# Kernel optimization log

Hardware: AMD Instinct MI355X
Metric: run time of the kernel (lower is better)

The kernel has to match this reference:

```python
import jax, jax.numpy as jnp
import numpy as np
from math import pi

BS, H, C = 4096, 1024, 512
H2, C2 = H // 2, C // 2


def _cm(x, y):
    # complex multiply with real/imag stored in last dim
    return jnp.stack([x[..., 0] * y[..., 0] - x[..., 1] * y[..., 1],
                      x[..., 0] * y[..., 1] + x[..., 1] * y[..., 0]], -1)


def _interleave(a, b):
    # (H2, C2),(H2, C2) -> (H, C2) rows [a0,b0,a1,b1,...]
    return jnp.stack([a, b], 1).reshape(-1, a.shape[1])


def _rotations(phi, theta):
    cp, sp = jnp.cos(phi), jnp.sin(phi)
    ct, st = jnp.cos(theta), jnp.sin(theta)
    z = jnp.zeros_like(ct)
    diag = jnp.stack([_interleave(cp * ct, ct), _interleave(sp * ct, z)], -1)      # (H, C2, 2)
    offd = jnp.stack([_interleave(-cp * st, st), _interleave(-sp * st, z)], -1)    # (H, C2, 2)
    return diag.transpose(1, 0, 2), offd.transpose(1, 0, 2)                        # (C2, H, 2)


def _swap_pairs(x):
    # swap elements within adjacent pairs along the hidden axis
    bs, h, _ = x.shape
    return x.reshape(bs, h // 2, 2, 2)[:, :, ::-1, :].reshape(bs, h, 2)


def setup_inputs() -> dict:
    key = jax.random.key(0)
    ks = jax.random.split(key, 5)
    x = jax.random.normal(ks[0], (BS, H, 2), dtype=jnp.float32)
    phi0 = 2 * pi * jax.random.normal(ks[1], (H2, C2), dtype=jnp.float32)
    theta0 = 2 * pi * jax.random.normal(ks[2], (H2, C2), dtype=jnp.float32)
    phi1 = 2 * pi * jax.random.normal(ks[3], (H2, C2), dtype=jnp.float32)
    theta1 = 2 * pi * jax.random.normal(ks[4], (H2, C2), dtype=jnp.float32)
    return {"x": x, "phi0": phi0, "theta0": theta0, "phi1": phi1, "theta1": theta1}


def reference(x, phi0, theta0, phi1, theta1):
    d0, o0 = _rotations(phi0, theta0)
    d1, o1 = _rotations(phi1, theta1)

    def step(xc, dd):
        dd0, oo0, dd1, oo1 = dd
        xc = _cm(xc, dd0) + _cm(_swap_pairs(xc), oo0)
        xc = jnp.roll(xc, -1, axis=1)   # cat(x[1:], x[:1])
        xc = _cm(xc, dd1) + _cm(_swap_pairs(xc), oo1)
        xc = jnp.roll(xc, 1, axis=1)    # cat(x[-1:], x[:-1])
        return xc, None

    x, _ = jax.lax.scan(step, x, (d0, o0, d1, o1))
    return x
```

## Files before the change

kernel.cpp:

```cpp
#include <hip/hip_runtime.h>


#define H_DIM 1024
#define C2 256
#define RPW 4


__global__ __launch_bounds__(256) void eunn_coef_kernel(
    const float* __restrict__ phi0, const float* __restrict__ theta0,
    const float* __restrict__ phi1, const float* __restrict__ theta1,
    float4* __restrict__ coef) {
    int t = blockIdx.x * 256 + threadIdx.x;
    int i = t & 511;
    int p = (t >> 9) & 1;
    int c = t >> 10;
    const float* phi   = p ? phi1   : phi0;
    const float* theta = p ? theta1 : theta0;
    float ph = phi[i * C2 + c];
    float th = theta[i * C2 + c];
    float sp, cp, st, ct;
    __sincosf(ph, &sp, &cp);
    __sincosf(th, &st, &ct);
    int j = i & 7;
    int l = i >> 3;
    coef[(((c * 2 + p) * 8) + j) * 64 + l] = make_float4(ct, st, cp, sp);
}

__device__ __forceinline__ void rot_pair(const float4 q,
                                         float& ur, float& ui,
                                         float& wr, float& wi) {
    float ar = fmaf(-q.y, wr, q.x * ur);
    float ai = fmaf(-q.y, wi, q.x * ui);
    float br = fmaf( q.x, wr, q.y * ur);
    float bi = fmaf( q.x, wi, q.y * ui);
    ur = fmaf(-q.w, ai, q.z * ar);
    ui = fmaf( q.w, ar, q.z * ai);
    wr = br;
    wi = bi;
}

__global__ __launch_bounds__(256, 1) void eunn_main_kernel(
    const float* __restrict__ x,
    const float4* __restrict__ coef,
    float* __restrict__ out) {
    const int lane = threadIdx.x & 63;
    const int wave = threadIdx.x >> 6;
    const int row0 = (blockIdx.x * 4 + wave) * RPW;
    const int lnext = (lane + 1) & 63;
    const int lprev = (lane + 63) & 63;

    float vr[RPW][16], vi[RPW][16];

#pragma unroll
    for (int r = 0; r < RPW; ++r) {
        const float4* src = (const float4*)(x + (size_t)(row0 + r) * (H_DIM * 2)) + lane * 8;
#pragma unroll
        for (int m = 0; m < 8; ++m) {
            float4 f = src[m];
            vr[r][2 * m]     = f.x; vi[r][2 * m]     = f.y;
            vr[r][2 * m + 1] = f.z; vi[r][2 * m + 1] = f.w;
        }
    }

    const float4* cl = coef + lane;

    float4 A[8], B[8];
#pragma unroll
    for (int j = 0; j < 8; ++j) A[j] = cl[j * 64];

#pragma unroll 1
    for (int c = 0; c < C2; ++c) {
        const float4* cb = cl + (size_t)c * 1024;

#pragma unroll
        for (int j = 0; j < 8; ++j) B[j] = cb[(8 + j) * 64];
        __builtin_amdgcn_sched_barrier(0);

#pragma unroll
        for (int j = 0; j < 8; ++j) {
#pragma unroll
            for (int r = 0; r < RPW; ++r)
                rot_pair(A[j], vr[r][2 * j],     vi[r][2 * j],
                               vr[r][2 * j + 1], vi[r][2 * j + 1]);
        }

        float4 qq = B[7];
        float qpx = __shfl(qq.x, lprev);
        float qpy = __shfl(qq.y, lprev);
        float nbr[RPW], nbi[RPW], pbr[RPW], pbi[RPW];
#pragma unroll
        for (int r = 0; r < RPW; ++r) {
            nbr[r] = __shfl(vr[r][0],  lnext);
            nbi[r] = __shfl(vi[r][0],  lnext);
            pbr[r] = __shfl(vr[r][15], lprev);
            pbi[r] = __shfl(vi[r][15], lprev);
        }

        const int cn = (c + 1 < C2) ? (c + 1) : 0;
        const float4* cnp = cl + (size_t)cn * 1024;
#pragma unroll
        for (int j = 0; j < 8; ++j) A[j] = cnp[j * 64];
        __builtin_amdgcn_sched_barrier(0);

#pragma unroll
        for (int j = 0; j < 7; ++j) {
#pragma unroll
            for (int r = 0; r < RPW; ++r)
                rot_pair(B[j], vr[r][2 * j + 1], vi[r][2 * j + 1],
                               vr[r][2 * j + 2], vi[r][2 * j + 2]);
        }

#pragma unroll
        for (int r = 0; r < RPW; ++r) {
            float ar = fmaf(-qq.y, nbr[r], qq.x * vr[r][15]);
            float ai = fmaf(-qq.y, nbi[r], qq.x * vi[r][15]);
            vr[r][15] = fmaf(-qq.w, ai, qq.z * ar);
            vi[r][15] = fmaf( qq.w, ar, qq.z * ai);
            float b0r = fmaf(qpx, vr[r][0], qpy * pbr[r]);
            float b0i = fmaf(qpx, vi[r][0], qpy * pbi[r]);
            vr[r][0] = b0r; vi[r][0] = b0i;
        }
    }

#pragma unroll
    for (int r = 0; r < RPW; ++r) {
        float4* dst = (float4*)(out + (size_t)(row0 + r) * (H_DIM * 2)) + lane * 8;
#pragma unroll
        for (int m = 0; m < 8; ++m) {
            dst[m] = make_float4(vr[r][2 * m],     vi[r][2 * m],
                                 vr[r][2 * m + 1], vi[r][2 * m + 1]);
        }
    }
}

extern "C" void kernel_launch(void* const* d_in, const int* in_sizes, int n_in,
                              void* d_out, int out_size, void* d_ws, size_t ws_size,
                              hipStream_t stream) {
    const float* x      = (const float*)d_in[0];
    const float* phi0   = (const float*)d_in[1];
    const float* theta0 = (const float*)d_in[2];
    const float* phi1   = (const float*)d_in[3];
    const float* theta1 = (const float*)d_in[4];
    float* out = (float*)d_out;
    float4* coef = (float4*)d_ws;

    hipLaunchKernelGGL(eunn_coef_kernel, dim3(1024), dim3(256), 0, stream,
                       phi0, theta0, phi1, theta1, coef);

    hipLaunchKernelGGL(eunn_main_kernel, dim3(256), dim3(256), 0, stream,
                       x, coef, out);
}
```

Before: 457.5 us.

## Halve rows per wave, double grid, and software-pipeline coefficient loads in groups

Each wave now processes two rows instead of four, and the grid doubles to 512 blocks with launch bounds allowing two blocks per CU, so more waves can hide latency. Coefficient loads are restructured into groups of four float4 loads issued ahead of the rotations that consume them, with empty asm pins and memory fences to enforce the ordering, and the first group for the next column is prefetched. The shuffles and boundary rotations are interleaved with independent work. This trades less per-wave coefficient reuse (each coefficient is loaded for fewer rows) for higher occupancy and finer-grained overlap of loads with math.

```diff
diff --git a/kernel.cpp b/kernel.cpp
--- a/kernel.cpp
+++ b/kernel.cpp
@@ -3,7 +3,7 @@
 
 #define H_DIM 1024
 #define C2 256
-#define RPW 4
+#define RPW 2
 
 
 __global__ __launch_bounds__(256) void eunn_coef_kernel(
@@ -39,7 +39,24 @@
     wi = bi;
 }
 
-__global__ __launch_bounds__(256, 1) void eunn_main_kernel(
+
+#define ROT2(q, e0, e1)                                                  \
+    do {                                                                 \
+        _Pragma("unroll")                                                \
+        for (int r = 0; r < RPW; ++r)                                    \
+            rot_pair(q, vr[r][e0], vi[r][e0], vr[r][e1], vi[r][e1]);     \
+    } while (0)
+
+#define PIN4(a, b, c, d)                                                 \
+    asm volatile(""                                                      \
+        : "+v"(a.x), "+v"(a.y), "+v"(a.z), "+v"(a.w),                    \
+          "+v"(b.x), "+v"(b.y), "+v"(b.z), "+v"(b.w),                    \
+          "+v"(c.x), "+v"(c.y), "+v"(c.z), "+v"(c.w),                    \
+          "+v"(d.x), "+v"(d.y), "+v"(d.z), "+v"(d.w))
+
+#define MEMFENCE asm volatile("" ::: "memory")
+
+__global__ __launch_bounds__(256, 2) void eunn_main_kernel(
     const float* __restrict__ x,
     const float4* __restrict__ coef,
     float* __restrict__ out) {
@@ -64,29 +81,21 @@
 
     const float4* cl = coef + lane;
 
-    float4 A[8], B[8];
-#pragma unroll
-    for (int j = 0; j < 8; ++j) A[j] = cl[j * 64];
+    float4 pA0 = cl[0 * 64], pA7 = cl[7 * 64], pQQ = cl[15 * 64], pA1 = cl[1 * 64];
 
 #pragma unroll 1
     for (int c = 0; c < C2; ++c) {
         const float4* cb = cl + (size_t)c * 1024;
+        const float4* cn = cl + (size_t)((c + 1) & (C2 - 1)) * 1024;
 
-#pragma unroll
-        for (int j = 0; j < 8; ++j) B[j] = cb[(8 + j) * 64];
-        __builtin_amdgcn_sched_barrier(0);
-
-#pragma unroll
-        for (int j = 0; j < 8; ++j) {
-#pragma unroll
-            for (int r = 0; r < RPW; ++r)
-                rot_pair(A[j], vr[r][2 * j],     vi[r][2 * j],
-                               vr[r][2 * j + 1], vi[r][2 * j + 1]);
-        }
-
-        float4 qq = B[7];
+        PIN4(pA0, pA7, pQQ, pA1);
+        float4 pA2 = cb[2 * 64], pA3 = cb[3 * 64], pA4 = cb[4 * 64], pA5 = cb[5 * 64];
+        MEMFENCE;
+        float4 qq = pQQ;
         float qpx = __shfl(qq.x, lprev);
         float qpy = __shfl(qq.y, lprev);
+        ROT2(pA0, 0, 1);
+        ROT2(pA7, 14, 15);
         float nbr[RPW], nbi[RPW], pbr[RPW], pbi[RPW];
 #pragma unroll
         for (int r = 0; r < RPW; ++r) {
@@ -95,20 +104,31 @@
             pbr[r] = __shfl(vr[r][15], lprev);
             pbi[r] = __shfl(vi[r][15], lprev);
         }
+        ROT2(pA1, 2, 3);
 
-        const int cn = (c + 1 < C2) ? (c + 1) : 0;
-        const float4* cnp = cl + (size_t)cn * 1024;
-#pragma unroll
-        for (int j = 0; j < 8; ++j) A[j] = cnp[j * 64];
-        __builtin_amdgcn_sched_barrier(0);
+        PIN4(pA2, pA3, pA4, pA5);
+        float4 pA6 = cb[6 * 64], pB0 = cb[8 * 64], pB1 = cb[9 * 64], pB2 = cb[10 * 64];
+        MEMFENCE;
+        ROT2(pA2, 4, 5);
+        ROT2(pA3, 6, 7);
+        ROT2(pA4, 8, 9);
+        ROT2(pA5, 10, 11);
 
-#pragma unroll
-        for (int j = 0; j < 7; ++j) {
-#pragma unroll
-            for (int r = 0; r < RPW; ++r)
-                rot_pair(B[j], vr[r][2 * j + 1], vi[r][2 * j + 1],
-                               vr[r][2 * j + 2], vi[r][2 * j + 2]);
-        }
+        PIN4(pA6, pB0, pB1, pB2);
+        float4 pB3 = cb[11 * 64], pB4 = cb[12 * 64], pB5 = cb[13 * 64], pB6 = cb[14 * 64];
+        MEMFENCE;
+        ROT2(pA6, 12, 13);
+        ROT2(pB0, 1, 2);
+        ROT2(pB1, 3, 4);
+        ROT2(pB2, 5, 6);
+
+        PIN4(pB3, pB4, pB5, pB6);
+        pA0 = cn[0 * 64]; pA7 = cn[7 * 64]; pQQ = cn[15 * 64]; pA1 = cn[1 * 64];
+        MEMFENCE;
+        ROT2(pB3, 7, 8);
+        ROT2(pB4, 9, 10);
+        ROT2(pB5, 11, 12);
+        ROT2(pB6, 13, 14);
 
 #pragma unroll
         for (int r = 0; r < RPW; ++r) {
@@ -147,6 +167,6 @@
     hipLaunchKernelGGL(eunn_coef_kernel, dim3(1024), dim3(256), 0, stream,
                        phi0, theta0, phi1, theta1, coef);
 
-    hipLaunchKernelGGL(eunn_main_kernel, dim3(256), dim3(256), 0, stream,
+    hipLaunchKernelGGL(eunn_main_kernel, dim3(512), dim3(256), 0, stream,
                        x, coef, out);
 }
```

After: 487.0 us. 1.06x slower.

## Split each row across two waves with LDS halo exchange per layer

Applied to the files above, without the earlier changes.

Each row of 1024 hidden elements is now split across two waves of 64 lanes, with 16 elements per lane. Each wave still processes 4 rows, and the grid grows to 1024 blocks of 128 threads. The boundary values at the wave edges are exchanged through shared memory, with a barrier every layer. The coefficient layout is reordered to match, and coefficient prefetch is double-buffered by unrolling two layers per loop. The aim is to raise the number of waves in flight and to halve per-thread register state, at the cost of an LDS exchange and a block barrier on every layer.

```diff
diff --git a/kernel.cpp b/kernel.cpp
--- a/kernel.cpp
+++ b/kernel.cpp
@@ -3,7 +3,6 @@
 
 #define H_DIM 1024
 #define C2 256
-#define RPW 4
 
 
 __global__ __launch_bounds__(256) void eunn_coef_kernel(
@@ -11,9 +10,12 @@
     const float* __restrict__ phi1, const float* __restrict__ theta1,
     float4* __restrict__ coef) {
     int t = blockIdx.x * 256 + threadIdx.x;
-    int i = t & 511;
-    int p = (t >> 9) & 1;
+    int l = t & 63;
+    int k = (t >> 6) & 3;
+    int p = (t >> 8) & 1;
+    int w = (t >> 9) & 1;
     int c = t >> 10;
+    int i = 256 * w + 4 * l + k;
     const float* phi   = p ? phi1   : phi0;
     const float* theta = p ? theta1 : theta0;
     float ph = phi[i * C2 + c];
@@ -21,9 +23,7 @@
     float sp, cp, st, ct;
     __sincosf(ph, &sp, &cp);
     __sincosf(th, &st, &ct);
-    int j = i & 7;
-    int l = i >> 3;
-    coef[(((c * 2 + p) * 8) + j) * 64 + l] = make_float4(ct, st, cp, sp);
+    coef[t] = make_float4(ct, st, cp, sp);
 }
 
 __device__ __forceinline__ void rot_pair(const float4 q,
@@ -39,96 +39,131 @@
     wi = bi;
 }
 
-__global__ __launch_bounds__(256, 1) void eunn_main_kernel(
+__global__ __launch_bounds__(128, 2) void eunn_main_kernel(
     const float* __restrict__ x,
     const float4* __restrict__ coef,
     float* __restrict__ out) {
     const int lane = threadIdx.x & 63;
-    const int wave = threadIdx.x >> 6;
-    const int row0 = (blockIdx.x * 4 + wave) * RPW;
+    const int w    = threadIdx.x >> 6;
+    const int row0 = blockIdx.x * 4;
     const int lnext = (lane + 1) & 63;
     const int lprev = (lane + 63) & 63;
 
-    float vr[RPW][16], vi[RPW][16];
+    __shared__ float4 ex[2][2][5];
+
+    float vr[4][8], vi[4][8];
 
 #pragma unroll
-    for (int r = 0; r < RPW; ++r) {
-        const float4* src = (const float4*)(x + (size_t)(row0 + r) * (H_DIM * 2)) + lane * 8;
+    for (int r = 0; r < 4; ++r) {
+        const float4* src = (const float4*)(x + (size_t)(row0 + r) * (H_DIM * 2))
+                            + (w * 256 + lane * 4);
 #pragma unroll
-        for (int m = 0; m < 8; ++m) {
-            float4 f = src[m];
-            vr[r][2 * m]     = f.x; vi[r][2 * m]     = f.y;
-            vr[r][2 * m + 1] = f.z; vi[r][2 * m + 1] = f.w;
+        for (int k = 0; k < 4; ++k) {
+            float4 f = src[k];
+            vr[r][2 * k]     = f.x; vi[r][2 * k]     = f.y;
+            vr[r][2 * k + 1] = f.z; vi[r][2 * k + 1] = f.w;
         }
     }
 
-    const float4* cl = coef + lane;
+    const float4* cl = coef + (w * 512 + lane);
 
-    float4 A[8], B[8];
+    float4 CA[4], CB[4], NA[4], NB[4];
 #pragma unroll
-    for (int j = 0; j < 8; ++j) A[j] = cl[j * 64];
+    for (int k = 0; k < 4; ++k) {
+        CA[k] = cl[k * 64];
+        CB[k] = cl[256 + k * 64];
+    }
+
+#define LAYER(CA_, CB_, NA_, NB_, cnext, par)                                      \
+    do {                                                                           \
+                    \
+        const float4* cn_ = cl + (size_t)(cnext) * 1024;                           \
+        _Pragma("unroll")                                                          \
+        for (int k = 0; k < 4; ++k) {                                              \
+            NA_[k] = cn_[k * 64];                                                  \
+            NB_[k] = cn_[256 + k * 64];                                            \
+        }                                                                          \
+        float4 qq = CB_[3];                                                        \
+        float qpx = __shfl(qq.x, lprev);                 \
+        float qpy = __shfl(qq.y, lprev);                 \
+                                        \
+        _Pragma("unroll")                                                          \
+        for (int k = 0; k < 4; ++k)                                                \
+            _Pragma("unroll")                                                      \
+            for (int r = 0; r < 4; ++r)                                            \
+                rot_pair(CA_[k], vr[r][2 * k],     vi[r][2 * k],                   \
+                                 vr[r][2 * k + 1], vi[r][2 * k + 1]);              \
+                 \
+        float nbr[4], nbi[4], pbr[4], pbi[4];                                      \
+        _Pragma("unroll")                                                          \
+        for (int r = 0; r < 4; ++r) {                                              \
+            nbr[r] = __shfl(vr[r][0], lnext);                                      \
+            nbi[r] = __shfl(vi[r][0], lnext);                                      \
+            pbr[r] = __shfl(vr[r][7], lprev);                                      \
+            pbi[r] = __shfl(vi[r][7], lprev);                                      \
+        }                                                                          \
+        if (lane == 0) {                                                           \
+            ex[par][w][0] = make_float4(vr[0][0], vi[0][0], vr[1][0], vi[1][0]);   \
+            ex[par][w][1] = make_float4(vr[2][0], vi[2][0], vr[3][0], vi[3][0]);   \
+        } else if (lane == 63) {                                                   \
+            ex[par][w][2] = make_float4(vr[0][7], vi[0][7], vr[1][7], vi[1][7]);   \
+            ex[par][w][3] = make_float4(vr[2][7], vi[2][7], vr[3][7], vi[3][7]);   \
+            ex[par][w][4] = make_float4(qq.x, qq.y, qq.x, qq.y);                   \
+        }                                                                          \
+              \
+        asm volatile("" ::: "memory");                                             \
+        asm volatile("s_waitcnt lgkmcnt(0)" ::: "memory");                         \
+        __builtin_amdgcn_s_barrier();                                              \
+        asm volatile("" ::: "memory");                                             \
+        {                                                                          \
+            float4 e0a = ex[par][w ^ 1][0], e0b = ex[par][w ^ 1][1];               \
+            float4 e7a = ex[par][w ^ 1][2], e7b = ex[par][w ^ 1][3];               \
+            float4 qpo = ex[par][w ^ 1][4];                                        \
+            if (lane == 63) {                                                      \
+                nbr[0] = e0a.x; nbi[0] = e0a.y; nbr[1] = e0a.z; nbi[1] = e0a.w;    \
+                nbr[2] = e0b.x; nbi[2] = e0b.y; nbr[3] = e0b.z; nbi[3] = e0b.w;    \
+            }                                                                      \
+            if (lane == 0) {                                                       \
+                pbr[0] = e7a.x; pbi[0] = e7a.y; pbr[1] = e7a.z; pbi[1] = e7a.w;    \
+                pbr[2] = e7b.x; pbi[2] = e7b.y; pbr[3] = e7b.z; pbi[3] = e7b.w;    \
+                qpx = qpo.x; qpy = qpo.y;                                          \
+            }                                                                      \
+        }                                                                          \
+                                 \
+        _Pragma("unroll")                                                          \
+        for (int k = 0; k < 3; ++k)                                                \
+            _Pragma("unroll")                                                      \
+            for (int r = 0; r < 4; ++r)                                            \
+                rot_pair(CB_[k], vr[r][2 * k + 1], vi[r][2 * k + 1],               \
+                                 vr[r][2 * k + 2], vi[r][2 * k + 2]);              \
+                                \
+        _Pragma("unroll")                                                          \
+        for (int r = 0; r < 4; ++r) {                                              \
+            float ar = fmaf(-qq.y, nbr[r], qq.x * vr[r][7]);                       \
+            float ai = fmaf(-qq.y, nbi[r], qq.x * vi[r][7]);                       \
+            vr[r][7] = fmaf(-qq.w, ai, qq.z * ar);                                 \
+            vi[r][7] = fmaf( qq.w, ar, qq.z * ai);                                 \
+            float b0r = fmaf(qpx, vr[r][0], qpy * pbr[r]);                         \
+            float b0i = fmaf(qpx, vi[r][0], qpy * pbi[r]);                         \
+            vr[r][0] = b0r; vi[r][0] = b0i;                                        \
+        }                                                                          \
+    } while (0)
 
 #pragma unroll 1
-    for (int c = 0; c < C2; ++c) {
-        const float4* cb = cl + (size_t)c * 1024;
+    for (int c = 0; c < C2; c += 2) {
+        LAYER(CA, CB, NA, NB, c + 1, 0);
+        LAYER(NA, NB, CA, CB, (c + 2) & (C2 - 1), 1);
+    }
+#undef LAYER
 
 #pragma unroll
-        for (int j = 0; j < 8; ++j) B[j] = cb[(8 + j) * 64];
-        __builtin_amdgcn_sched_barrier(0);
-
+    for (int r = 0; r < 4; ++r) {
+        float4* dst = (float4*)(out + (size_t)(row0 + r) * (H_DIM * 2))
+                      + (w * 256 + lane * 4);
 #pragma unroll
-        for (int j = 0; j < 8; ++j) {
-#pragma unroll
-            for (int r = 0; r < RPW; ++r)
-                rot_pair(A[j], vr[r][2 * j],     vi[r][2 * j],
-                               vr[r][2 * j + 1], vi[r][2 * j + 1]);
-        }
-
-        float4 qq = B[7];
-        float qpx = __shfl(qq.x, lprev);
-        float qpy = __shfl(qq.y, lprev);
-        float nbr[RPW], nbi[RPW], pbr[RPW], pbi[RPW];
-#pragma unroll
-        for (int r = 0; r < RPW; ++r) {
-            nbr[r] = __shfl(vr[r][0],  lnext);
-            nbi[r] = __shfl(vi[r][0],  lnext);
-            pbr[r] = __shfl(vr[r][15], lprev);
-            pbi[r] = __shfl(vi[r][15], lprev);
-        }
-
-        const int cn = (c + 1 < C2) ? (c + 1) : 0;
-        const float4* cnp = cl + (size_t)cn * 1024;
-#pragma unroll
-        for (int j = 0; j < 8; ++j) A[j] = cnp[j * 64];
-        __builtin_amdgcn_sched_barrier(0);
-
-#pragma unroll
-        for (int j = 0; j < 7; ++j) {
-#pragma unroll
-            for (int r = 0; r < RPW; ++r)
-                rot_pair(B[j], vr[r][2 * j + 1], vi[r][2 * j + 1],
-                               vr[r][2 * j + 2], vi[r][2 * j + 2]);
-        }
-
-#pragma unroll
-        for (int r = 0; r < RPW; ++r) {
-            float ar = fmaf(-qq.y, nbr[r], qq.x * vr[r][15]);
-            float ai = fmaf(-qq.y, nbi[r], qq.x * vi[r][15]);
-            vr[r][15] = fmaf(-qq.w, ai, qq.z * ar);
-            vi[r][15] = fmaf( qq.w, ar, qq.z * ai);
-            float b0r = fmaf(qpx, vr[r][0], qpy * pbr[r]);
-            float b0i = fmaf(qpx, vi[r][0], qpy * pbi[r]);
-            vr[r][0] = b0r; vi[r][0] = b0i;
-        }
-    }
-
-#pragma unroll
-    for (int r = 0; r < RPW; ++r) {
-        float4* dst = (float4*)(out + (size_t)(row0 + r) * (H_DIM * 2)) + lane * 8;
-#pragma unroll
-        for (int m = 0; m < 8; ++m) {
-            dst[m] = make_float4(vr[r][2 * m],     vi[r][2 * m],
-                                 vr[r][2 * m + 1], vi[r][2 * m + 1]);
+        for (int k = 0; k < 4; ++k) {
+            dst[k] = make_float4(vr[r][2 * k],     vi[r][2 * k],
+                                 vr[r][2 * k + 1], vi[r][2 * k + 1]);
         }
     }
 }
@@ -147,6 +182,6 @@
     hipLaunchKernelGGL(eunn_coef_kernel, dim3(1024), dim3(256), 0, stream,
                        phi0, theta0, phi1, theta1, coef);
 
-    hipLaunchKernelGGL(eunn_main_kernel, dim3(256), dim3(256), 0, stream,
+    hipLaunchKernelGGL(eunn_main_kernel, dim3(1024), dim3(128), 0, stream,
                        x, coef, out);
 }
```

After: 465.9 us. About the same (+1.8%).

## Halve rows per wave, double grid, and software-pipeline coef loads with inline asm

Applied to the files above, without the earlier changes.

Each wave now holds 2 rows instead of 4 and the grid doubles to 512 blocks, with waves_per_eu set to 2 so more waves are resident to hide latency. Coefficient loads are issued through inline-asm global_load_dwordx4 with immediate offsets and explicit vmcnt(0) drains. The next layer's loads overlap the current layer's rotation math, and the boundary shuffles are issued early between rotations. The trade-off is that each coefficient load is now amortised over fewer rows, which raises coefficient traffic, and the hand-placed waitcnts could serialise work.

```diff
diff --git a/kernel.cpp b/kernel.cpp
--- a/kernel.cpp
+++ b/kernel.cpp
@@ -3,7 +3,9 @@
 
 #define H_DIM 1024
 #define C2 256
-#define RPW 4
+#define RPW 2
+
+typedef float f4 __attribute__((ext_vector_type(4)));
 
 
 __global__ __launch_bounds__(256) void eunn_coef_kernel(
@@ -26,7 +28,7 @@
     coef[(((c * 2 + p) * 8) + j) * 64 + l] = make_float4(ct, st, cp, sp);
 }
 
-__device__ __forceinline__ void rot_pair(const float4 q,
+__device__ __forceinline__ void rot_pair(const f4 q,
                                          float& ur, float& ui,
                                          float& wr, float& wi) {
     float ar = fmaf(-q.y, wr, q.x * ur);
@@ -39,9 +41,28 @@
     wi = bi;
 }
 
-__global__ __launch_bounds__(256, 1) void eunn_main_kernel(
+#define GLOAD(dst, base, off)                                              \
+    asm volatile("global_load_dwordx4 %0, %1, off offset:" #off            \
+                 : "=v"(dst) : "v"(base))
+
+#define VMDRAIN                                                            \
+    do {                                                                   \
+        asm volatile("s_waitcnt vmcnt(0)");                                \
+        __builtin_amdgcn_sched_barrier(0);                                 \
+    } while (0)
+
+#define ROT2(q, e0, e1)                                                    \
+    do {                                                                   \
+        _Pragma("unroll")                                                  \
+        for (int r = 0; r < RPW; ++r)                                      \
+            rot_pair(q, vr[r][e0], vi[r][e0], vr[r][e1], vi[r][e1]);       \
+    } while (0)
+
+__global__ __launch_bounds__(256)
+__attribute__((amdgpu_waves_per_eu(2, 2)))
+void eunn_main_kernel(
     const float* __restrict__ x,
-    const float4* __restrict__ coef,
+    const f4* __restrict__ coef,
     float* __restrict__ out) {
     const int lane = threadIdx.x & 63;
     const int wave = threadIdx.x >> 6;
@@ -53,40 +74,42 @@
 
 #pragma unroll
     for (int r = 0; r < RPW; ++r) {
-        const float4* src = (const float4*)(x + (size_t)(row0 + r) * (H_DIM * 2)) + lane * 8;
+        const f4* src = (const f4*)(x + (size_t)(row0 + r) * (H_DIM * 2)) + lane * 8;
 #pragma unroll
         for (int m = 0; m < 8; ++m) {
-            float4 f = src[m];
+            f4 f = src[m];
             vr[r][2 * m]     = f.x; vi[r][2 * m]     = f.y;
             vr[r][2 * m + 1] = f.z; vi[r][2 * m + 1] = f.w;
         }
     }
 
-    const float4* cl = coef + lane;
+    const f4* cl = coef + lane;
 
-    float4 A[8], B[8];
-#pragma unroll
-    for (int j = 0; j < 8; ++j) A[j] = cl[j * 64];
+    f4 A0, A1, A2, A3, A4, A5, A6, A7;
+    f4 B0, B1, B2, B3, B4, B5, B6, B7;
+
+    {
+        const f4* g0 = cl;
+        const f4* g1 = cl + 256;
+        GLOAD(A0, g0, 0); GLOAD(A1, g0, 1024); GLOAD(A2, g0, 2048); GLOAD(A3, g0, 3072);
+        GLOAD(A4, g1, 0); GLOAD(A5, g1, 1024); GLOAD(A6, g1, 2048); GLOAD(A7, g1, 3072);
+    }
+    VMDRAIN;
 
 #pragma unroll 1
     for (int c = 0; c < C2; ++c) {
-        const float4* cb = cl + (size_t)c * 1024;
+        const f4* cb = cl + (size_t)c * 1024;
+        const f4* cn = cl + (size_t)((c + 1) & (C2 - 1)) * 1024;
 
-#pragma unroll
-        for (int j = 0; j < 8; ++j) B[j] = cb[(8 + j) * 64];
-        __builtin_amdgcn_sched_barrier(0);
-
-#pragma unroll
-        for (int j = 0; j < 8; ++j) {
-#pragma unroll
-            for (int r = 0; r < RPW; ++r)
-                rot_pair(A[j], vr[r][2 * j],     vi[r][2 * j],
-                               vr[r][2 * j + 1], vi[r][2 * j + 1]);
+        {
+            const f4* g2 = cb + 512;
+            const f4* g3 = cb + 768;
+            GLOAD(B0, g2, 0); GLOAD(B1, g2, 1024); GLOAD(B2, g2, 2048); GLOAD(B3, g2, 3072);
+            GLOAD(B4, g3, 0); GLOAD(B5, g3, 1024); GLOAD(B6, g3, 2048); GLOAD(B7, g3, 3072);
         }
 
-        float4 qq = B[7];
-        float qpx = __shfl(qq.x, lprev);
-        float qpy = __shfl(qq.y, lprev);
+        ROT2(A0, 0, 1);
+        ROT2(A7, 14, 15);
         float nbr[RPW], nbi[RPW], pbr[RPW], pbi[RPW];
 #pragma unroll
         for (int r = 0; r < RPW; ++r) {
@@ -95,40 +118,56 @@
             pbr[r] = __shfl(vr[r][15], lprev);
             pbi[r] = __shfl(vi[r][15], lprev);
         }
+        ROT2(A1, 2, 3);
+        ROT2(A2, 4, 5);
+        ROT2(A3, 6, 7);
+        ROT2(A4, 8, 9);
+        ROT2(A5, 10, 11);
+        ROT2(A6, 12, 13);
 
-        const int cn = (c + 1 < C2) ? (c + 1) : 0;
-        const float4* cnp = cl + (size_t)cn * 1024;
-#pragma unroll
-        for (int j = 0; j < 8; ++j) A[j] = cnp[j * 64];
-        __builtin_amdgcn_sched_barrier(0);
+        VMDRAIN;
 
-#pragma unroll
-        for (int j = 0; j < 7; ++j) {
-#pragma unroll
-            for (int r = 0; r < RPW; ++r)
-                rot_pair(B[j], vr[r][2 * j + 1], vi[r][2 * j + 1],
-                               vr[r][2 * j + 2], vi[r][2 * j + 2]);
+        float qpx = __shfl(B7.x, lprev);
+        float qpy = __shfl(B7.y, lprev);
+
+        {
+            const f4* g0 = cn;
+            const f4* g1 = cn + 256;
+            GLOAD(A0, g0, 0); GLOAD(A1, g0, 1024); GLOAD(A2, g0, 2048); GLOAD(A3, g0, 3072);
+            GLOAD(A4, g1, 0); GLOAD(A5, g1, 1024); GLOAD(A6, g1, 2048); GLOAD(A7, g1, 3072);
         }
+
+        ROT2(B0, 1, 2);
+        ROT2(B1, 3, 4);
+        ROT2(B2, 5, 6);
+        ROT2(B3, 7, 8);
+        ROT2(B4, 9, 10);
+        ROT2(B5, 11, 12);
+        ROT2(B6, 13, 14);
 
 #pragma unroll
         for (int r = 0; r < RPW; ++r) {
-            float ar = fmaf(-qq.y, nbr[r], qq.x * vr[r][15]);
-            float ai = fmaf(-qq.y, nbi[r], qq.x * vi[r][15]);
-            vr[r][15] = fmaf(-qq.w, ai, qq.z * ar);
-            vi[r][15] = fmaf( qq.w, ar, qq.z * ai);
+            float ar = fmaf(-B7.y, nbr[r], B7.x * vr[r][15]);
+            float ai = fmaf(-B7.y, nbi[r], B7.x * vi[r][15]);
+            vr[r][15] = fmaf(-B7.w, ai, B7.z * ar);
+            vi[r][15] = fmaf( B7.w, ar, B7.z * ai);
             float b0r = fmaf(qpx, vr[r][0], qpy * pbr[r]);
             float b0i = fmaf(qpx, vi[r][0], qpy * pbi[r]);
             vr[r][0] = b0r; vi[r][0] = b0i;
         }
+
+        VMDRAIN;
     }
 
 #pragma unroll
     for (int r = 0; r < RPW; ++r) {
-        float4* dst = (float4*)(out + (size_t)(row0 + r) * (H_DIM * 2)) + lane * 8;
+        f4* dst = (f4*)(out + (size_t)(row0 + r) * (H_DIM * 2)) + lane * 8;
 #pragma unroll
         for (int m = 0; m < 8; ++m) {
-            dst[m] = make_float4(vr[r][2 * m],     vi[r][2 * m],
-                                 vr[r][2 * m + 1], vi[r][2 * m + 1]);
+            f4 o;
+            o.x = vr[r][2 * m];     o.y = vi[r][2 * m];
+            o.z = vr[r][2 * m + 1]; o.w = vi[r][2 * m + 1];
+            dst[m] = o;
         }
     }
 }
@@ -147,6 +186,6 @@
     hipLaunchKernelGGL(eunn_coef_kernel, dim3(1024), dim3(256), 0, stream,
                        phi0, theta0, phi1, theta1, coef);
 
-    hipLaunchKernelGGL(eunn_main_kernel, dim3(256), dim3(256), 0, stream,
-                       x, coef, out);
+    hipLaunchKernelGGL(eunn_main_kernel, dim3(512), dim3(256), 0, stream,
+                       x, (const f4*)coef, out);
 }
```

Result: slower. 466.7 us (+2.0%).
